# Kernel tuning notes

Measured on AMD Instinct MI355X. Metric: run time of the kernel, lower is better.

Reference implementation:

```python
import jax, jax.numpy as jnp
import numpy as np

N_NODES = 100000
N_EDGES = 1600000


def setup_inputs() -> dict:
    key = jax.random.key(0)
    k1, k2, k3, k4 = jax.random.split(key, 4)
    x = jax.random.normal(k1, (N_NODES, 128), dtype=jnp.float32)
    edge_idx = jax.random.randint(k2, (2, N_EDGES), 0, N_NODES, dtype=jnp.int64)
    W1 = jax.random.normal(k3, (128, 64), dtype=jnp.float32) * (1.0 / np.sqrt(128))
    b1 = jnp.zeros((64,), dtype=jnp.float32)
    W2 = jax.random.normal(k4, (64, 40), dtype=jnp.float32) * (1.0 / np.sqrt(64))
    b2 = jnp.zeros((40,), dtype=jnp.float32)
    return {"x": x, "edge_idx": edge_idx, "W1": W1, "b1": b1, "W2": W2, "b2": b2}


def _gcn_conv(x, src, dst, norm, W, b, n_nodes):
    # x @ W -> gather by src, scale by symmetric norm, scatter-add to dst, + bias
    h = x @ W                               # [N, d_out]
    msg = h[src] * norm[:, None]            # [E+N, d_out]
    out = jax.ops.segment_sum(msg, dst, num_segments=n_nodes)
    return out + b


def _norm_and_loops(edge_idx, n_nodes):
    # PyG GCNConv default: add self-loops, norm = deg^-1/2[src] * deg^-1/2[dst]
    loops = jnp.arange(n_nodes, dtype=edge_idx.dtype)
    src = jnp.concatenate([edge_idx[0], loops])
    dst = jnp.concatenate([edge_idx[1], loops])
    deg = jnp.zeros((n_nodes,), jnp.float32).at[dst].add(1.0)
    dinv = jnp.where(deg > 0, jax.lax.rsqrt(deg), 0.0)
    norm = dinv[src] * dinv[dst]
    return src, dst, norm


def reference(x, edge_idx, W1, b1, W2, b2):
    n_nodes = x.shape[0]
    src, dst, norm = _norm_and_loops(edge_idx, n_nodes)
    hidden = jax.nn.relu(_gcn_conv(x, src, dst, norm, W1, b1, n_nodes))
    # dropout is a no-op in eval mode (training=False)
    return _gcn_conv(hidden, src, dst, norm, W2, b2, n_nodes)
```

## Files before the change

kernel.cpp:

```cpp
#include <hip/hip_runtime.h>

#define D_IN  128
#define D_HID 64
#define D_OUT 40

static __device__ __forceinline__ unsigned short f2bf(float f) {
    unsigned int u = __float_as_uint(f);
    unsigned int r = (u + 0x7fffu + ((u >> 16) & 1u)) >> 16;
    return (unsigned short)r;
}
static __device__ __forceinline__ float bflo(unsigned int u) {
    return __uint_as_float(u << 16);
}
static __device__ __forceinline__ float bfhi(unsigned int u) {
    return __uint_as_float(u & 0xffff0000u);
}

__global__ __launch_bounds__(256) void k_deg(const int* __restrict__ dst,
                                             unsigned int* __restrict__ cnt,
                                             unsigned int* __restrict__ rank, int E) {
    int e = blockIdx.x * 256 + threadIdx.x;
    if (e < E) rank[e] = atomicAdd(&cnt[dst[e]], 1u);
}

__global__ __launch_bounds__(256) void k_scan1(const unsigned int* __restrict__ deg,
                                               unsigned int* __restrict__ off,
                                               unsigned int* __restrict__ bsum,
                                               float* __restrict__ dinv, int N) {
    __shared__ unsigned int s[256];
    const int tid = threadIdx.x;
    const int i = blockIdx.x * 256 + tid;
    unsigned int v = (i < N) ? deg[i] : 0u;
    if (i < N) dinv[i] = rsqrtf((float)(v + 1u));
    s[tid] = v;
    __syncthreads();
    for (int d = 1; d < 256; d <<= 1) {
        unsigned int t = (tid >= d) ? s[tid - d] : 0u;
        __syncthreads();
        s[tid] += t;
        __syncthreads();
    }
    if (i < N) off[i] = s[tid] - v;
    if (tid == 255) bsum[blockIdx.x] = s[tid];
}

__global__ __launch_bounds__(512) void k_scan2(unsigned int* __restrict__ bsum, int NB) {
    __shared__ unsigned int s[512];
    const int tid = threadIdx.x;
    unsigned int v = (tid < NB) ? bsum[tid] : 0u;
    s[tid] = v;
    __syncthreads();
    for (int d = 1; d < 512; d <<= 1) {
        unsigned int t = (tid >= d) ? s[tid - d] : 0u;
        __syncthreads();
        s[tid] += t;
        __syncthreads();
    }
    if (tid < NB) bsum[tid] = s[tid] - v;
}

__global__ __launch_bounds__(256) void k_scan3(unsigned int* __restrict__ off,
                                               const unsigned int* __restrict__ bsum,
                                               int N, int E) {
    int i = blockIdx.x * 256 + threadIdx.x;
    if (i < N) off[i] += bsum[blockIdx.x];
    if (i == 0) off[N] = (unsigned int)E;
}

__global__ __launch_bounds__(256) void k_fill(const int* __restrict__ src,
                                              const int* __restrict__ dst,
                                              const unsigned int* __restrict__ off,
                                              const unsigned int* __restrict__ rank,
                                              int* __restrict__ csr_src, int E) {
    int e = blockIdx.x * 256 + threadIdx.x;
    if (e >= E) return;
    csr_src[off[dst[e]] + rank[e]] = src[e];
}

__global__ __launch_bounds__(256) void k_gemm1(const float* __restrict__ x,
                                               const float* __restrict__ W1,
                                               const float* __restrict__ dinv,
                                               unsigned short* __restrict__ h1s, int N) {
    __shared__ float w[D_IN * D_HID];
    __shared__ float xs[16][D_IN + 4];
    const int tid = threadIdx.x;
    const float4* W4 = (const float4*)W1;
    float4* w4 = (float4*)w;
    for (int i = tid; i < D_IN * D_HID / 4; i += 256) w4[i] = W4[i];
    const int row0 = blockIdx.x * 16;
    const float4* X4 = (const float4*)(x + (size_t)row0 * D_IN);
    for (int i = tid; i < 16 * D_IN / 4; i += 256) {
        float4 v = X4[i];
        int r = i >> 5;
        int k = (i & 31) * 4;
        *(float4*)&xs[r][k] = v;
    }
    __syncthreads();
    const int r  = tid >> 4;
    const int c4 = (tid & 15) * 4;
    float a0 = 0, a1 = 0, a2 = 0, a3 = 0;
#pragma unroll 8
    for (int k = 0; k < D_IN; ++k) {
        float  xv = xs[r][k];
        float4 wv = *(const float4*)&w[k * D_HID + c4];
        a0 = fmaf(xv, wv.x, a0);
        a1 = fmaf(xv, wv.y, a1);
        a2 = fmaf(xv, wv.z, a2);
        a3 = fmaf(xv, wv.w, a3);
    }
    const int row = row0 + r;
    if (row < N) {
        float dv = dinv[row];
        uint2 o;
        o.x = (unsigned)f2bf(a0 * dv) | ((unsigned)f2bf(a1 * dv) << 16);
        o.y = (unsigned)f2bf(a2 * dv) | ((unsigned)f2bf(a3 * dv) << 16);
        *(uint2*)&h1s[(size_t)row * D_HID + c4] = o;
    }
}

__global__ __launch_bounds__(320) void k_gemm2(const float* __restrict__ hid,
                                               const float* __restrict__ W2,
                                               const float* __restrict__ dinv,
                                               unsigned short* __restrict__ h2s, int N) {
    __shared__ float w[D_HID * D_OUT];
    __shared__ float xs[16][D_HID + 4];
    const int tid = threadIdx.x;
    const float2* W22 = (const float2*)W2;
    float2* w2 = (float2*)w;
    for (int i = tid; i < D_HID * D_OUT / 2; i += 320) w2[i] = W22[i];
    const int row0 = blockIdx.x * 16;
    const float4* X4 = (const float4*)(hid + (size_t)row0 * D_HID);
    for (int i = tid; i < 16 * D_HID / 4; i += 320) {
        float4 v = X4[i];
        int r = i >> 4;
        int k = (i & 15) * 4;
        *(float4*)&xs[r][k] = v;
    }
    __syncthreads();
    const int r  = tid / 20;
    const int c2 = (tid % 20) * 2;
    float a0 = 0, a1 = 0;
#pragma unroll 8
    for (int k = 0; k < D_HID; ++k) {
        float  xv = xs[r][k];
        float2 wv = *(const float2*)&w[k * D_OUT + c2];
        a0 = fmaf(xv, wv.x, a0);
        a1 = fmaf(xv, wv.y, a1);
    }
    const int row = row0 + r;
    if (row < N) {
        float dv = dinv[row];
        unsigned int o = (unsigned)f2bf(a0 * dv) | ((unsigned)f2bf(a1 * dv) << 16);
        *(unsigned int*)&h2s[(size_t)row * D_OUT + c2] = o;
    }
}

__global__ __launch_bounds__(256) void k_gather1(const unsigned int* __restrict__ off,
                                                 const int* __restrict__ csr_src,
                                                 const unsigned int* __restrict__ h1s,
                                                 const float* __restrict__ dinv,
                                                 const float* __restrict__ b1,
                                                 float* __restrict__ hidden, int N) {
    const int gtid = blockIdx.x * 256 + threadIdx.x;
    const int wid2 = gtid >> 6;
    const int lane = threadIdx.x & 63;
    const int half = lane >> 5;
    const int hl   = lane & 31;
    const int node = wid2 * 2 + half;
    if (node >= N) return;
    const int start = (int)off[node];
    const int end   = (int)off[node + 1];
    unsigned int u = h1s[(size_t)node * 32 + hl];
    float a0 = bflo(u), a1 = bfhi(u);
    for (int base = start; base < end; base += 32) {
        const int nb = min(32, end - base);
        int sv = (base + hl < end) ? csr_src[base + hl] : 0;
        int j = 0;
        for (; j + 3 < nb; j += 4) {
            int s0 = __shfl(sv, j, 32),     s1 = __shfl(sv, j + 1, 32);
            int s2 = __shfl(sv, j + 2, 32), s3 = __shfl(sv, j + 3, 32);
            unsigned int u0 = h1s[(size_t)s0 * 32 + hl];
            unsigned int u1 = h1s[(size_t)s1 * 32 + hl];
            unsigned int u2 = h1s[(size_t)s2 * 32 + hl];
            unsigned int u3 = h1s[(size_t)s3 * 32 + hl];
            a0 += (bflo(u0) + bflo(u1)) + (bflo(u2) + bflo(u3));
            a1 += (bfhi(u0) + bfhi(u1)) + (bfhi(u2) + bfhi(u3));
        }
        for (; j < nb; ++j) {
            int s = __shfl(sv, j, 32);
            unsigned int uu = h1s[(size_t)s * 32 + hl];
            a0 += bflo(uu);
            a1 += bfhi(uu);
        }
    }
    const float dv = dinv[node];
    const float2 bb = *(const float2*)&b1[hl * 2];
    float v0 = dv * a0 + bb.x;
    float v1 = dv * a1 + bb.y;
    float2 o = {v0 > 0.0f ? v0 : 0.0f, v1 > 0.0f ? v1 : 0.0f};
    *(float2*)&hidden[(size_t)node * D_HID + hl * 2] = o;
}

__global__ __launch_bounds__(256) void k_gather2(const unsigned int* __restrict__ off,
                                                 const int* __restrict__ csr_src,
                                                 const unsigned int* __restrict__ h2s,
                                                 const float* __restrict__ dinv,
                                                 const float* __restrict__ b2,
                                                 float* __restrict__ out, int N) {
    const int gtid = blockIdx.x * 256 + threadIdx.x;
    const int wid2 = gtid >> 6;
    const int lane = threadIdx.x & 63;
    const int half = lane >> 5;
    const int hl   = lane & 31;
    const int node = wid2 * 2 + half;
    if (node >= N) return;
    const int start = (int)off[node];
    const int end   = (int)off[node + 1];
    const bool act = hl < 20;
    float a0 = 0.0f, a1 = 0.0f;
    if (act) {
        unsigned int u = h2s[(size_t)node * 20 + hl];
        a0 = bflo(u); a1 = bfhi(u);
    }
    for (int base = start; base < end; base += 32) {
        const int nb = min(32, end - base);
        int sv = (base + hl < end) ? csr_src[base + hl] : 0;
        int j = 0;
        for (; j + 3 < nb; j += 4) {
            int s0 = __shfl(sv, j, 32),     s1 = __shfl(sv, j + 1, 32);
            int s2 = __shfl(sv, j + 2, 32), s3 = __shfl(sv, j + 3, 32);
            if (act) {
                unsigned int u0 = h2s[(size_t)s0 * 20 + hl];
                unsigned int u1 = h2s[(size_t)s1 * 20 + hl];
                unsigned int u2 = h2s[(size_t)s2 * 20 + hl];
                unsigned int u3 = h2s[(size_t)s3 * 20 + hl];
                a0 += (bflo(u0) + bflo(u1)) + (bflo(u2) + bflo(u3));
                a1 += (bfhi(u0) + bfhi(u1)) + (bfhi(u2) + bfhi(u3));
            }
        }
        for (; j < nb; ++j) {
            int s = __shfl(sv, j, 32);
            if (act) {
                unsigned int uu = h2s[(size_t)s * 20 + hl];
                a0 += bflo(uu);
                a1 += bfhi(uu);
            }
        }
    }
    if (act) {
        const float dv = dinv[node];
        const float2 bb = *(const float2*)&b2[hl * 2];
        float2 o = {dv * a0 + bb.x, dv * a1 + bb.y};
        *(float2*)&out[(size_t)node * D_OUT + hl * 2] = o;
    }
}

extern "C" void kernel_launch(void* const* d_in, const int* in_sizes, int n_in,
                              void* d_out, int out_size, void* d_ws, size_t ws_size,
                              hipStream_t stream) {
    const float* x  = (const float*)d_in[0];
    const int*  eix = (const int*)d_in[1];
    const float* W1 = (const float*)d_in[2];
    const float* b1 = (const float*)d_in[3];
    const float* W2 = (const float*)d_in[4];
    const float* b2 = (const float*)d_in[5];
    float* out = (float*)d_out;

    const int N = in_sizes[0] / D_IN;
    const int E = in_sizes[1] / 2;
    const int* src = eix;
    const int* dst = eix + E;
    const int NB = (N + 255) / 256;

    char* ws = (char*)d_ws;
    size_t off_b = 0;
    auto alloc = [&](size_t bytes) {
        void* p = ws + off_b;
        off_b = (off_b + bytes + 255) & ~(size_t)255;
        return p;
    };
    unsigned int*   deg     = (unsigned int*)alloc((size_t)N * 4);
    float*          dinv    = (float*)alloc((size_t)N * 4);
    unsigned int*   offsets = (unsigned int*)alloc((size_t)(N + 1) * 4);
    unsigned int*   bsums   = (unsigned int*)alloc(512 * 4);
    int*            csr_src = (int*)alloc((size_t)E * 4);
    unsigned short* h1s     = (unsigned short*)alloc((size_t)N * D_HID * 2);
    float*          hidden  = (float*)alloc((size_t)N * D_HID * 4);
    unsigned short* h2s     = h1s;
    unsigned int*   rank    = (unsigned int*)hidden;

    hipMemsetAsync(deg, 0, (size_t)N * 4, stream);

    k_deg  <<<(E + 255) / 256, 256, 0, stream>>>(dst, deg, rank, E);
    k_scan1<<<NB, 256, 0, stream>>>(deg, offsets, bsums, dinv, N);
    k_scan2<<<1, 512, 0, stream>>>(bsums, NB);
    k_scan3<<<NB, 256, 0, stream>>>(offsets, bsums, N, E);
    k_fill <<<(E + 255) / 256, 256, 0, stream>>>(src, dst, offsets, rank, csr_src, E);

    const int gwaves = (N + 1) / 2;
    const int gblocks = (gwaves + 3) / 4;

    k_gemm1  <<<(N + 15) / 16, 256, 0, stream>>>(x, W1, dinv, h1s, N);
    k_gather1<<<gblocks, 256, 0, stream>>>(offsets, csr_src, (const unsigned int*)h1s, dinv, b1, hidden, N);

    k_gemm2  <<<(N + 15) / 16, 320, 0, stream>>>(hidden, W2, dinv, h2s, N);
    k_gather2<<<gblocks, 256, 0, stream>>>(offsets, csr_src, (const unsigned int*)h2s, dinv, b2, out, N);
}
```

Measured before the change: 340.2 us.

## Fuse degree count with GEMM1 and gather1 with GEMM2

Merges the degree-count atomics and the first GEMM into one launch by splitting blocks by index, so GEMM1 no longer depends on dinv and stores unscaled bf16. The source-side normalization moves into gather1, which now loads dinv per neighbor. Gather1 is fused with GEMM2 through shared memory, which removes the fp32 hidden buffer write and read and one launch. In exchange, every edge now does an extra dinv lookup, and the bigger fused blocks may have lower occupancy.

```diff
diff --git a/kernel.cpp b/kernel.cpp
--- a/kernel.cpp
+++ b/kernel.cpp
@@ -16,78 +16,24 @@
     return __uint_as_float(u & 0xffff0000u);
 }
 
-__global__ __launch_bounds__(256) void k_deg(const int* __restrict__ dst,
-                                             unsigned int* __restrict__ cnt,
-                                             unsigned int* __restrict__ rank, int E) {
-    int e = blockIdx.x * 256 + threadIdx.x;
-    if (e < E) rank[e] = atomicAdd(&cnt[dst[e]], 1u);
-}
-
-__global__ __launch_bounds__(256) void k_scan1(const unsigned int* __restrict__ deg,
-                                               unsigned int* __restrict__ off,
-                                               unsigned int* __restrict__ bsum,
-                                               float* __restrict__ dinv, int N) {
-    __shared__ unsigned int s[256];
-    const int tid = threadIdx.x;
-    const int i = blockIdx.x * 256 + tid;
-    unsigned int v = (i < N) ? deg[i] : 0u;
-    if (i < N) dinv[i] = rsqrtf((float)(v + 1u));
-    s[tid] = v;
-    __syncthreads();
-    for (int d = 1; d < 256; d <<= 1) {
-        unsigned int t = (tid >= d) ? s[tid - d] : 0u;
-        __syncthreads();
-        s[tid] += t;
-        __syncthreads();
-    }
-    if (i < N) off[i] = s[tid] - v;
-    if (tid == 255) bsum[blockIdx.x] = s[tid];
-}
-
-__global__ __launch_bounds__(512) void k_scan2(unsigned int* __restrict__ bsum, int NB) {
-    __shared__ unsigned int s[512];
-    const int tid = threadIdx.x;
-    unsigned int v = (tid < NB) ? bsum[tid] : 0u;
-    s[tid] = v;
-    __syncthreads();
-    for (int d = 1; d < 512; d <<= 1) {
-        unsigned int t = (tid >= d) ? s[tid - d] : 0u;
-        __syncthreads();
-        s[tid] += t;
-        __syncthreads();
-    }
-    if (tid < NB) bsum[tid] = s[tid] - v;
-}
-
-__global__ __launch_bounds__(256) void k_scan3(unsigned int* __restrict__ off,
-                                               const unsigned int* __restrict__ bsum,
-                                               int N, int E) {
-    int i = blockIdx.x * 256 + threadIdx.x;
-    if (i < N) off[i] += bsum[blockIdx.x];
-    if (i == 0) off[N] = (unsigned int)E;
-}
-
-__global__ __launch_bounds__(256) void k_fill(const int* __restrict__ src,
-                                              const int* __restrict__ dst,
-                                              const unsigned int* __restrict__ off,
-                                              const unsigned int* __restrict__ rank,
-                                              int* __restrict__ csr_src, int E) {
-    int e = blockIdx.x * 256 + threadIdx.x;
-    if (e >= E) return;
-    csr_src[off[dst[e]] + rank[e]] = src[e];
-}
-
-__global__ __launch_bounds__(256) void k_gemm1(const float* __restrict__ x,
-                                               const float* __restrict__ W1,
-                                               const float* __restrict__ dinv,
-                                               unsigned short* __restrict__ h1s, int N) {
+__global__ __launch_bounds__(256) void k_deg_g1(const int* __restrict__ dst,
+                                                unsigned int* __restrict__ cnt,
+                                                unsigned int* __restrict__ rank, int E, int DB,
+                                                const float* __restrict__ x,
+                                                const float* __restrict__ W1,
+                                                unsigned short* __restrict__ h1s, int N) {
     __shared__ float w[D_IN * D_HID];
     __shared__ float xs[16][D_IN + 4];
+    if ((int)blockIdx.x < DB) {
+        int e = blockIdx.x * 256 + threadIdx.x;
+        if (e < E) rank[e] = atomicAdd(&cnt[dst[e]], 1u);
+        return;
+    }
     const int tid = threadIdx.x;
     const float4* W4 = (const float4*)W1;
     float4* w4 = (float4*)w;
     for (int i = tid; i < D_IN * D_HID / 4; i += 256) w4[i] = W4[i];
-    const int row0 = blockIdx.x * 16;
+    const int row0 = (blockIdx.x - DB) * 16;
     const float4* X4 = (const float4*)(x + (size_t)row0 * D_IN);
     for (int i = tid; i < 16 * D_IN / 4; i += 256) {
         float4 v = X4[i];
@@ -110,68 +56,100 @@
     }
     const int row = row0 + r;
     if (row < N) {
-        float dv = dinv[row];
         uint2 o;
-        o.x = (unsigned)f2bf(a0 * dv) | ((unsigned)f2bf(a1 * dv) << 16);
-        o.y = (unsigned)f2bf(a2 * dv) | ((unsigned)f2bf(a3 * dv) << 16);
+        o.x = (unsigned)f2bf(a0) | ((unsigned)f2bf(a1) << 16);
+        o.y = (unsigned)f2bf(a2) | ((unsigned)f2bf(a3) << 16);
         *(uint2*)&h1s[(size_t)row * D_HID + c4] = o;
     }
 }
 
-__global__ __launch_bounds__(320) void k_gemm2(const float* __restrict__ hid,
-                                               const float* __restrict__ W2,
-                                               const float* __restrict__ dinv,
-                                               unsigned short* __restrict__ h2s, int N) {
-    __shared__ float w[D_HID * D_OUT];
-    __shared__ float xs[16][D_HID + 4];
+__global__ __launch_bounds__(256) void k_scan1(const unsigned int* __restrict__ deg,
+                                               unsigned int* __restrict__ off,
+                                               unsigned int* __restrict__ bsum,
+                                               float* __restrict__ dinv, int N) {
+    __shared__ unsigned int s[256];
     const int tid = threadIdx.x;
-    const float2* W22 = (const float2*)W2;
-    float2* w2 = (float2*)w;
-    for (int i = tid; i < D_HID * D_OUT / 2; i += 320) w2[i] = W22[i];
-    const int row0 = blockIdx.x * 16;
-    const float4* X4 = (const float4*)(hid + (size_t)row0 * D_HID);
-    for (int i = tid; i < 16 * D_HID / 4; i += 320) {
-        float4 v = X4[i];
-        int r = i >> 4;
-        int k = (i & 15) * 4;
-        *(float4*)&xs[r][k] = v;
-    }
-    __syncthreads();
-    const int r  = tid / 20;
-    const int c2 = (tid % 20) * 2;
-    float a0 = 0, a1 = 0;
-#pragma unroll 8
-    for (int k = 0; k < D_HID; ++k) {
-        float  xv = xs[r][k];
-        float2 wv = *(const float2*)&w[k * D_OUT + c2];
-        a0 = fmaf(xv, wv.x, a0);
-        a1 = fmaf(xv, wv.y, a1);
-    }
-    const int row = row0 + r;
-    if (row < N) {
-        float dv = dinv[row];
-        unsigned int o = (unsigned)f2bf(a0 * dv) | ((unsigned)f2bf(a1 * dv) << 16);
-        *(unsigned int*)&h2s[(size_t)row * D_OUT + c2] = o;
-    }
-}
-
-__global__ __launch_bounds__(256) void k_gather1(const unsigned int* __restrict__ off,
-                                                 const int* __restrict__ csr_src,
-                                                 const unsigned int* __restrict__ h1s,
-                                                 const float* __restrict__ dinv,
-                                                 const float* __restrict__ b1,
-                                                 float* __restrict__ hidden, int N) {
-    const int gtid = blockIdx.x * 256 + threadIdx.x;
-    const int wid2 = gtid >> 6;
-    const int lane = threadIdx.x & 63;
+    const int i = blockIdx.x * 256 + tid;
+    unsigned int v = (i < N) ? deg[i] : 0u;
+    if (i < N) dinv[i] = rsqrtf((float)(v + 1u));
+    s[tid] = v;
+    __syncthreads();
+    for (int d = 1; d < 256; d <<= 1) {
+        unsigned int t = (tid >= d) ? s[tid - d] : 0u;
+        __syncthreads();
+        s[tid] += t;
+        __syncthreads();
+    }
+    if (i < N) off[i] = s[tid] - v;
+    if (tid == 255) bsum[blockIdx.x] = s[tid];
+}
+
+__global__ __launch_bounds__(512) void k_scan2(unsigned int* __restrict__ bsum, int NB) {
+    __shared__ unsigned int s[512];
+    const int tid = threadIdx.x;
+    unsigned int v = (tid < NB) ? bsum[tid] : 0u;
+    s[tid] = v;
+    __syncthreads();
+    for (int d = 1; d < 512; d <<= 1) {
+        unsigned int t = (tid >= d) ? s[tid - d] : 0u;
+        __syncthreads();
+        s[tid] += t;
+        __syncthreads();
+    }
+    if (tid < NB) bsum[tid] = s[tid] - v;
+}
+
+__global__ __launch_bounds__(256) void k_scan3(unsigned int* __restrict__ off,
+                                               const unsigned int* __restrict__ bsum,
+                                               int N, int E) {
+    int i = blockIdx.x * 256 + threadIdx.x;
+    if (i < N) off[i] += bsum[blockIdx.x];
+    if (i == 0) off[N] = (unsigned int)E;
+}
+
+__global__ __launch_bounds__(256) void k_fill(const int* __restrict__ src,
+                                              const int* __restrict__ dst,
+                                              const unsigned int* __restrict__ off,
+                                              const unsigned int* __restrict__ rank,
+                                              int* __restrict__ csr_src, int E) {
+    int e = blockIdx.x * 256 + threadIdx.x;
+    if (e >= E) return;
+    csr_src[off[dst[e]] + rank[e]] = src[e];
+}
+
+__global__ __launch_bounds__(256) void k_g1g2(const unsigned int* __restrict__ off,
+                                              const int* __restrict__ csr_src,
+                                              const unsigned int* __restrict__ h1s,
+                                              const float* __restrict__ dinv,
+                                              const float* __restrict__ b1,
+                                              const float* __restrict__ W2,
+                                              unsigned short* __restrict__ h2s, int N) {
+    __shared__ float w2s[D_HID * D_OUT];
+    __shared__ float hrow[8][D_HID];
+    const int tid = threadIdx.x;
+    const float4* W4 = (const float4*)W2;
+    float4* w4 = (float4*)w2s;
+    for (int i = tid; i < D_HID * D_OUT / 4; i += 256) w4[i] = W4[i];
+    __syncthreads();
+
+    const int lane = tid & 63;
     const int half = lane >> 5;
     const int hl   = lane & 31;
-    const int node = wid2 * 2 + half;
-    if (node >= N) return;
-    const int start = (int)off[node];
-    const int end   = (int)off[node + 1];
-    unsigned int u = h1s[(size_t)node * 32 + hl];
-    float a0 = bflo(u), a1 = bfhi(u);
+    const int slot = (tid >> 6) * 2 + half;
+    const int node = blockIdx.x * 8 + slot;
+    const bool valid = node < N;
+
+    int start = 0, end = 0;
+    float a0 = 0.0f, a1 = 0.0f;
+    float dn = 0.0f;
+    if (valid) {
+        start = (int)off[node];
+        end   = (int)off[node + 1];
+        dn = dinv[node];
+        unsigned int u = h1s[(size_t)node * 32 + hl];
+        a0 = dn * bflo(u);
+        a1 = dn * bfhi(u);
+    }
     for (int base = start; base < end; base += 32) {
         const int nb = min(32, end - base);
         int sv = (base + hl < end) ? csr_src[base + hl] : 0;
@@ -179,26 +157,44 @@
         for (; j + 3 < nb; j += 4) {
             int s0 = __shfl(sv, j, 32),     s1 = __shfl(sv, j + 1, 32);
             int s2 = __shfl(sv, j + 2, 32), s3 = __shfl(sv, j + 3, 32);
-            unsigned int u0 = h1s[(size_t)s0 * 32 + hl];
-            unsigned int u1 = h1s[(size_t)s1 * 32 + hl];
-            unsigned int u2 = h1s[(size_t)s2 * 32 + hl];
-            unsigned int u3 = h1s[(size_t)s3 * 32 + hl];
-            a0 += (bflo(u0) + bflo(u1)) + (bflo(u2) + bflo(u3));
-            a1 += (bfhi(u0) + bfhi(u1)) + (bfhi(u2) + bfhi(u3));
+            unsigned int u0 = h1s[(size_t)s0 * 32 + hl]; float d0 = dinv[s0];
+            unsigned int u1 = h1s[(size_t)s1 * 32 + hl]; float d1 = dinv[s1];
+            unsigned int u2 = h1s[(size_t)s2 * 32 + hl]; float d2 = dinv[s2];
+            unsigned int u3 = h1s[(size_t)s3 * 32 + hl]; float d3 = dinv[s3];
+            a0 = fmaf(d0, bflo(u0), a0); a1 = fmaf(d0, bfhi(u0), a1);
+            a0 = fmaf(d1, bflo(u1), a0); a1 = fmaf(d1, bfhi(u1), a1);
+            a0 = fmaf(d2, bflo(u2), a0); a1 = fmaf(d2, bfhi(u2), a1);
+            a0 = fmaf(d3, bflo(u3), a0); a1 = fmaf(d3, bfhi(u3), a1);
         }
         for (; j < nb; ++j) {
             int s = __shfl(sv, j, 32);
             unsigned int uu = h1s[(size_t)s * 32 + hl];
-            a0 += bflo(uu);
-            a1 += bfhi(uu);
-        }
-    }
-    const float dv = dinv[node];
-    const float2 bb = *(const float2*)&b1[hl * 2];
-    float v0 = dv * a0 + bb.x;
-    float v1 = dv * a1 + bb.y;
-    float2 o = {v0 > 0.0f ? v0 : 0.0f, v1 > 0.0f ? v1 : 0.0f};
-    *(float2*)&hidden[(size_t)node * D_HID + hl * 2] = o;
+            float dd = dinv[s];
+            a0 = fmaf(dd, bflo(uu), a0);
+            a1 = fmaf(dd, bfhi(uu), a1);
+        }
+    }
+    if (valid) {
+        const float2 bb = *(const float2*)&b1[hl * 2];
+        float v0 = fmaf(dn, a0, bb.x);
+        float v1 = fmaf(dn, a1, bb.y);
+        hrow[slot][hl * 2]     = v0 > 0.0f ? v0 : 0.0f;
+        hrow[slot][hl * 2 + 1] = v1 > 0.0f ? v1 : 0.0f;
+    }
+    __syncthreads();
+    if (valid && hl < 20) {
+        const int c2 = hl * 2;
+        float s0 = 0.0f, s1 = 0.0f;
+#pragma unroll 8
+        for (int k = 0; k < D_HID; ++k) {
+            float  xv = hrow[slot][k];
+            float2 wv = *(const float2*)&w2s[k * D_OUT + c2];
+            s0 = fmaf(xv, wv.x, s0);
+            s1 = fmaf(xv, wv.y, s1);
+        }
+        unsigned int o = (unsigned)f2bf(s0 * dn) | ((unsigned)f2bf(s1 * dn) << 16);
+        *(unsigned int*)&h2s[(size_t)node * D_OUT + c2] = o;
+    }
 }
 
 __global__ __launch_bounds__(256) void k_gather2(const unsigned int* __restrict__ off,
@@ -250,7 +246,7 @@
     if (act) {
         const float dv = dinv[node];
         const float2 bb = *(const float2*)&b2[hl * 2];
-        float2 o = {dv * a0 + bb.x, dv * a1 + bb.y};
+        float2 o = {fmaf(dv, a0, bb.x), fmaf(dv, a1, bb.y)};
         *(float2*)&out[(size_t)node * D_OUT + hl * 2] = o;
     }
 }
@@ -285,24 +281,26 @@
     unsigned int*   bsums   = (unsigned int*)alloc(512 * 4);
     int*            csr_src = (int*)alloc((size_t)E * 4);
     unsigned short* h1s     = (unsigned short*)alloc((size_t)N * D_HID * 2);
-    float*          hidden  = (float*)alloc((size_t)N * D_HID * 4);
-    unsigned short* h2s     = h1s;
-    unsigned int*   rank    = (unsigned int*)hidden;
+    unsigned short* h2s     = (unsigned short*)alloc((size_t)E >= (size_t)N * D_OUT / 2
+                                                     ? (size_t)E * 4 : (size_t)N * D_OUT * 2);
+    unsigned int*   rank    = (unsigned int*)h2s;
 
     hipMemsetAsync(deg, 0, (size_t)N * 4, stream);
 
-    k_deg  <<<(E + 255) / 256, 256, 0, stream>>>(dst, deg, rank, E);
+    const int DB = (E + 255) / 256;
+    const int GB = (N + 15) / 16;
+
+    k_deg_g1<<<DB + GB, 256, 0, stream>>>(dst, deg, rank, E, DB, x, W1, h1s, N);
+
     k_scan1<<<NB, 256, 0, stream>>>(deg, offsets, bsums, dinv, N);
     k_scan2<<<1, 512, 0, stream>>>(bsums, NB);
     k_scan3<<<NB, 256, 0, stream>>>(offsets, bsums, N, E);
     k_fill <<<(E + 255) / 256, 256, 0, stream>>>(src, dst, offsets, rank, csr_src, E);
 
+    k_g1g2  <<<(N + 7) / 8, 256, 0, stream>>>(offsets, csr_src, (const unsigned int*)h1s,
+                                              dinv, b1, W2, h2s, N);
     const int gwaves = (N + 1) / 2;
     const int gblocks = (gwaves + 3) / 4;
-
-    k_gemm1  <<<(N + 15) / 16, 256, 0, stream>>>(x, W1, dinv, h1s, N);
-    k_gather1<<<gblocks, 256, 0, stream>>>(offsets, csr_src, (const unsigned int*)h1s, dinv, b1, hidden, N);
-
-    k_gemm2  <<<(N + 15) / 16, 320, 0, stream>>>(hidden, W2, dinv, h2s, N);
-    k_gather2<<<gblocks, 256, 0, stream>>>(offsets, csr_src, (const unsigned int*)h2s, dinv, b2, out, N);
-}
+    k_gather2<<<gblocks, 256, 0, stream>>>(offsets, csr_src, (const unsigned int*)h2s,
+                                           dinv, b2, out, N);
+}
```

New measurement: 328.2 us. -3.5%, faster.
